# Kernel tuning notes

Hardware: AMD Instinct MI355X
Metric: run time of the kernel (lower is better)

## Reference

```python
import jax, jax.numpy as jnp
import numpy as np

S1 = (42, 1600, 1408); S2 = (21, 800, 704); S3 = (11, 400, 352); S4 = (6, 200, 176)
OFF = np.array([[dz, dy, dx] for dz in (-1, 0, 1) for dy in (-1, 0, 1) for dx in (-1, 0, 1)], np.int64)
KOFF = np.array([[kz, ky, kx] for kz in (0, 1, 2) for ky in (0, 1, 2) for kx in (0, 1, 2)], np.int64)

def _keys(c, s):
    return (c[:, 0] * s[1] + c[:, 1]) * s[2] + c[:, 2]

def _lookup(skeys, qk, valid):
    pos = np.searchsorted(skeys, qk)
    posc = np.clip(pos, 0, len(skeys) - 1)
    found = valid & (skeys[posc] == qk)
    return np.where(found, posc, -1).astype(np.int32)

def _subm_nbr(coords, skeys, shape):
    N = len(coords); nbr = np.empty((N, 27), np.int32); sh = np.array(shape)
    for t in range(27):
        q = coords + OFF[t]
        valid = np.all((q >= 0) & (q < sh), axis=1)
        nbr[:, t] = _lookup(skeys, _keys(q, shape), valid)
    return nbr

def _inv_nbr(fcoords, ckeys, cshape):
    # inverse of stride-2, pad-1, k-3 sparse conv: coarse = (fine + 1 - k) / 2
    N = len(fcoords); nbr = np.empty((N, 27), np.int32); csh = np.array(cshape)
    for t in range(27):
        cand = fcoords + 1 - KOFF[t]
        valid = np.all(cand >= 0, axis=1) & np.all(cand % 2 == 0, axis=1)
        cc = cand // 2
        valid &= np.all(cc < csh, axis=1)
        nbr[:, t] = _lookup(ckeys, _keys(cc, cshape), valid)
    return nbr

def _geometry():
    rng = np.random.default_rng(0)
    n = 130000
    c = np.stack([rng.integers(0, S1[i], n) for i in range(3)], 1).astype(np.int64)
    uk, idx = np.unique(_keys(c, S1), return_index=True)
    c1 = c[idx][:100000]; k1 = uk[:len(c1)]
    def down(cf, s):
        cc = cf // 2
        uk, idx = np.unique(_keys(cc, s), return_index=True)
        return cc[idx], uk
    c2, k2 = down(c1, S2); c3, k3 = down(c2, S3); c4, k4 = down(c3, S4)
    return dict(nbr4=_subm_nbr(c4, k4, S4), inv43=_inv_nbr(c3, k4, S4),
                nbr3=_subm_nbr(c3, k3, S3), inv32=_inv_nbr(c2, k3, S3),
                nbr2=_subm_nbr(c2, k2, S2), inv21=_inv_nbr(c1, k2, S2),
                nbr1=_subm_nbr(c1, k1, S1), n4=len(c4), n1=len(c1))

_SPECS = [("m4", 64, 64), ("i4", 64, 64), ("m3", 64, 64), ("i3", 64, 32),
          ("m2", 32, 32), ("i2", 32, 16), ("m1", 16, 16), ("c5", 16, 3)]

def _params(key):
    p = {}
    for i, (nm, ci, co) in enumerate(_SPECS):
        k = jax.random.fold_in(key, i)
        p["W_" + nm] = jax.random.normal(k, (27, ci, co), jnp.float32) * (1.0 / np.sqrt(27.0 * ci))
        p["g_" + nm] = jnp.ones((co,), jnp.float32)
        p["b_" + nm] = jnp.zeros((co,), jnp.float32)
    return p

def setup_inputs() -> dict:
    geo = _geometry()
    key = jax.random.key(0)
    inp = {k: jnp.asarray(v) for k, v in geo.items() if k.startswith(("nbr", "inv"))}
    inp["x"] = jax.random.normal(jax.random.fold_in(key, 100), (geo["n4"], 64), jnp.float32)
    inp.update(_params(key))
    return inp

def _block(f, nbr, W, g, b, relu=True):
    # gather-GEMM (sparse conv), then BatchNorm1d (training mode, eps=1e-3), then ReLU
    m = nbr >= 0                                             # [N,27]
    x = jnp.where(m[..., None], f[jnp.maximum(nbr, 0)], 0.0)  # [N,27,Cin]
    y = jnp.einsum('nkc,kcd->nd', x, W)                      # [N,Cout]
    mu = y.mean(0); var = y.var(0)
    y = (y - mu) * jax.lax.rsqrt(var + 1e-3) * g + b
    return jax.nn.relu(y) if relu else y

def reference(x, nbr4, inv43, nbr3, inv32, nbr2, inv21, nbr1,
              W_m4, g_m4, b_m4, W_i4, g_i4, b_i4, W_m3, g_m3, b_m3, W_i3, g_i3, b_i3,
              W_m2, g_m2, b_m2, W_i2, g_i2, b_i2, W_m1, g_m1, b_m1, W_c5, g_c5, b_c5):
    h = _block(x, nbr4, W_m4, g_m4, b_m4)      # subm4: [N4,64]
    h = _block(h, inv43, W_i4, g_i4, b_i4)     # inverse conv4 -> [N3,64]
    h = _block(h, nbr3, W_m3, g_m3, b_m3)      # subm3
    h = _block(h, inv32, W_i3, g_i3, b_i3)     # inverse conv3 -> [N2,32]
    h = _block(h, nbr2, W_m2, g_m2, b_m2)      # subm2
    h = _block(h, inv21, W_i2, g_i2, b_i2)     # inverse conv2 -> [N1,16]
    h = _block(h, nbr1, W_m1, g_m1, b_m1)      # subm1
    return _block(h, nbr1, W_c5, g_c5, b_c5, relu=False)  # conv5 (shares subm1 rulebook), BN only
```

## Files before the change

### kernel.cpp

```cpp
#include <hip/hip_runtime.h>

typedef _Float16 HALF;
typedef _Float16 f16x8 __attribute__((ext_vector_type(8)));
typedef float f32x4 __attribute__((ext_vector_type(4)));
typedef int i32x4 __attribute__((ext_vector_type(4)));

struct WArgs { const float* W[8]; HALF* dst[8]; };

__global__ void convert_all_w_kernel(WArgs a)
{
    const int CIs[8]  = {64, 64, 64, 64, 32, 32, 16, 16};
    const int COs[8]  = {64, 64, 64, 32, 32, 16, 16, 3};
    const int COPs[8] = {64, 64, 64, 32, 32, 16, 16, 16};
    const int L = blockIdx.y;
    const int CI = CIs[L], CO = COs[L], COP = COPs[L];
    const int K = 27 * CI, KP = (K + 31) & ~31;
    const int total = COP * KP;
    for (int i = blockIdx.x * 256 + threadIdx.x; i < total; i += gridDim.x * 256) {
        int jp = i / KP;
        int kp = i - jp * KP;
        float v = (jp < CO && kp < K) ? a.W[L][(size_t)kp * CO + jp] : 0.f;
        a.dst[L][((size_t)(kp >> 5) * COP + jp) * 32 + (kp & 31)] = (HALF)v;
    }
}

__global__ void convert_x_kernel(const float* __restrict__ x, HALF* __restrict__ xh, int total)
{
    int i = blockIdx.x * 256 + threadIdx.x;
    if (i < total) xh[i] = (HALF)x[i];
}

template<int CO_PAD, bool FUSED>
__global__ __launch_bounds__(256, 2) void conv_static(
    const HALF* __restrict__ h, const int* __restrict__ nbr,
    const HALF* __restrict__ Wt, HALF* __restrict__ yout,
    float* __restrict__ sums, int n,
    const float* __restrict__ psums, const float* __restrict__ pg,
    const float* __restrict__ pb, float pinvn)
{
    constexpr int CI   = 64;
    constexpr int NMT  = 2;
    constexpr int NJB  = CO_PAD / 16;
    constexpr int NCB  = 2;
    constexpr int ROWS = 32;
    constexpr int PAIRS = NMT * NJB;
    constexpr int TPW  = 7;

    __shared__ f32x4 lred[2][PAIRS * 64];
    __shared__ float lscbi[2][64];

    const int wv   = threadIdx.x >> 6;
    const int lane = threadIdx.x & 63;
    const int l15  = lane & 15;
    const int lq   = lane >> 4;

    int bid = blockIdx.x;
    {
        const int nwg = gridDim.x;
        const int q = nwg >> 3, r = nwg & 7;
        const int xcd = bid & 7, idx = bid >> 3;
        bid = (xcd < r ? xcd * (q + 1) : r * (q + 1) + (xcd - r) * q) + idx;
    }
    const int rowBase = bid * ROWS;

    if constexpr (FUSED) {
        const int c = threadIdx.x;
        if (c < CI) {
            float s = 0.f, q = 0.f;
#pragma unroll
            for (int k = 0; k < 8; ++k) { s += psums[k * 128 + c]; q += psums[k * 128 + CI + c]; }
            const float mu  = s * pinvn;
            const float var = q * pinvn - mu * mu;
            const float sc  = rsqrtf(var + 1e-3f) * pg[c];
            lscbi[0][c] = sc;
            lscbi[1][c] = pb[c] - mu * sc;
        }
    }

    f32x4 acc[NMT][NJB];
#pragma unroll
    for (int mt = 0; mt < NMT; ++mt)
#pragma unroll
        for (int jb = 0; jb < NJB; ++jb)
#pragma unroll
            for (int r = 0; r < 4; ++r) acc[mt][jb][r] = 0.f;

    int  nbo[NMT];
    bool rok[NMT];
#pragma unroll
    for (int mt = 0; mt < NMT; ++mt) {
        const int row = rowBase + mt * 16 + l15;
        rok[mt] = row < n;
        nbo[mt] = min(row, n - 1) * 27;
    }

    if constexpr (FUSED) __syncthreads();

    f16x8 sc8[NCB], bi8[NCB];
    if constexpr (FUSED) {
#pragma unroll
        for (int cb = 0; cb < NCB; ++cb) {
            const int c0 = cb * 32 + ((lq * 8) & (CI - 1));
#pragma unroll
            for (int j = 0; j < 8; ++j) {
                sc8[cb][j] = (HALF)lscbi[0][c0 + j];
                bi8[cb][j] = (HALF)lscbi[1][c0 + j];
            }
        }
    }

    const int t0 = wv * TPW;

    int   ipf[2][NMT];
    f16x8 apf[2][NMT][2];
#pragma unroll
    for (int p = 0; p < 2; ++p) {
        const int t = t0 + p;
#pragma unroll
        for (int mt = 0; mt < NMT; ++mt) {
            const int v   = nbr[nbo[mt] + (t < 27 ? t : 26)];
            const int idx = (rok[mt] && t < 27) ? v : -1;
            ipf[p][mt] = idx;
            const HALF* pa = h + ((max(idx, 0) << 6) + lq * 8);
            apf[p][mt][0] = *(const f16x8*)(pa);
            apf[p][mt][1] = *(const f16x8*)(pa + 32);
        }
    }

#pragma unroll
    for (int tt = 0; tt < TPW; ++tt) {
        const int t = t0 + tt;
        if (t >= 27) break;
        const int cur = tt & 1;

        f16x8 a0[NMT], a1[NMT]; int im[NMT];
#pragma unroll
        for (int mt = 0; mt < NMT; ++mt) {
            a0[mt] = apf[cur][mt][0]; a1[mt] = apf[cur][mt][1]; im[mt] = ipf[cur][mt];
        }

        if (tt + 2 < TPW && t + 2 < 27) {
#pragma unroll
            for (int mt = 0; mt < NMT; ++mt) {
                const int v   = nbr[nbo[mt] + t + 2];
                const int idx = rok[mt] ? v : -1;
                ipf[cur][mt] = idx;
                const HALF* pa = h + ((max(idx, 0) << 6) + lq * 8);
                apf[cur][mt][0] = *(const f16x8*)(pa);
                apf[cur][mt][1] = *(const f16x8*)(pa + 32);
            }
        }

        const HALF* wb = Wt + (size_t)(2 * t) * (CO_PAD * 32) + lq * 8;
        f16x8 b0[NJB], b1[NJB];
#pragma unroll
        for (int jb = 0; jb < NJB; ++jb) {
            b0[jb] = *(const f16x8*)(wb + (size_t)(jb * 16 + l15) * 32);
            b1[jb] = *(const f16x8*)(wb + CO_PAD * 32 + (size_t)(jb * 16 + l15) * 32);
        }

#pragma unroll
        for (int mt = 0; mt < NMT; ++mt) {
            f16x8 a = a0[mt];
            if constexpr (FUSED) {
                a = a * sc8[0] + bi8[0];
#pragma unroll
                for (int j = 0; j < 8; ++j) a[j] = (a[j] < (HALF)0.f) ? (HALF)0.f : a[j];
            }
            const int m = ~(im[mt] >> 31);
            i32x4 ai = __builtin_bit_cast(i32x4, a);
            ai.x &= m; ai.y &= m; ai.z &= m; ai.w &= m;
            a = __builtin_bit_cast(f16x8, ai);
#pragma unroll
            for (int jb = 0; jb < NJB; ++jb)
                acc[mt][jb] = __builtin_amdgcn_mfma_f32_16x16x32_f16(a, b0[jb], acc[mt][jb], 0, 0, 0);
        }
#pragma unroll
        for (int mt = 0; mt < NMT; ++mt) {
            f16x8 a = a1[mt];
            if constexpr (FUSED) {
                a = a * sc8[1] + bi8[1];
#pragma unroll
                for (int j = 0; j < 8; ++j) a[j] = (a[j] < (HALF)0.f) ? (HALF)0.f : a[j];
            }
            const int m = ~(im[mt] >> 31);
            i32x4 ai = __builtin_bit_cast(i32x4, a);
            ai.x &= m; ai.y &= m; ai.z &= m; ai.w &= m;
            a = __builtin_bit_cast(f16x8, ai);
#pragma unroll
            for (int jb = 0; jb < NJB; ++jb)
                acc[mt][jb] = __builtin_amdgcn_mfma_f32_16x16x32_f16(a, b1[jb], acc[mt][jb], 0, 0, 0);
        }
    }

    if (wv & 1) {
#pragma unroll
        for (int mt = 0; mt < NMT; ++mt)
#pragma unroll
            for (int jb = 0; jb < NJB; ++jb)
                lred[wv >> 1][(mt * NJB + jb) * 64 + lane] = acc[mt][jb];
    }
    __syncthreads();
    if (!(wv & 1)) {
#pragma unroll
        for (int mt = 0; mt < NMT; ++mt)
#pragma unroll
            for (int jb = 0; jb < NJB; ++jb)
                acc[mt][jb] += lred[wv >> 1][(mt * NJB + jb) * 64 + lane];
    }
    __syncthreads();
    if (wv == 2) {
#pragma unroll
        for (int mt = 0; mt < NMT; ++mt)
#pragma unroll
            for (int jb = 0; jb < NJB; ++jb)
                lred[0][(mt * NJB + jb) * 64 + lane] = acc[mt][jb];
    }
    __syncthreads();

    if (wv == 0) {
#pragma unroll
        for (int mt = 0; mt < NMT; ++mt)
#pragma unroll
            for (int jb = 0; jb < NJB; ++jb)
                acc[mt][jb] += lred[0][(mt * NJB + jb) * 64 + lane];

        float* sl = sums + (bid & 7) * 128;
#pragma unroll
        for (int jb = 0; jb < NJB; ++jb) {
            const int col = jb * 16 + l15;
            float s = 0.f, sq = 0.f;
#pragma unroll
            for (int mt = 0; mt < NMT; ++mt) {
                const int rb = rowBase + mt * 16 + lq * 4;
#pragma unroll
                for (int r = 0; r < 4; ++r) {
                    if (rb + r < n) {
                        const float v = acc[mt][jb][r];
                        yout[(size_t)(rb + r) * CO_PAD + col] = (HALF)v;
                        s += v;
                        sq += v * v;
                    }
                }
            }
            s  += __shfl_xor(s, 16);  s  += __shfl_xor(s, 32);
            sq += __shfl_xor(sq, 16); sq += __shfl_xor(sq, 32);
            if (lane < 16) {
                atomicAdd(&sl[col], s);
                atomicAdd(&sl[CO_PAD + col], sq);
            }
        }
    }
}

template<int CI, int CO_PAD, bool FUSED>
__global__ __launch_bounds__(256, 2) void conv_dyn(
    const HALF* __restrict__ h, const int* __restrict__ nbr,
    const HALF* __restrict__ Wt, HALF* __restrict__ yout,
    float* __restrict__ sums, int n,
    const float* __restrict__ psums, const float* __restrict__ pg,
    const float* __restrict__ pb, float pinvn)
{
    constexpr int NMT   = 2;
    constexpr int NJB   = CO_PAD / 16;
    constexpr int NCB   = (CI >= 64) ? 2 : 1;
    constexpr int ROWS  = 32;
    constexpr int PAIRS = NMT * NJB;

    __shared__ f32x4 lred[2][PAIRS * 64];
    __shared__ float lscbi[2][64];
    __shared__ int   lidx[ROWS * 27];
    __shared__ int   tflag[27];
    __shared__ int   tls[32];
    __shared__ int   ntapS;

    const int wv   = threadIdx.x >> 6;
    const int lane = threadIdx.x & 63;
    const int l15  = lane & 15;
    const int lq   = lane >> 4;

    int bid = blockIdx.x;
    {
        const int nwg = gridDim.x;
        const int q = nwg >> 3, r = nwg & 7;
        const int xcd = bid & 7, idx = bid >> 3;
        bid = (xcd < r ? xcd * (q + 1) : r * (q + 1) + (xcd - r) * q) + idx;
    }
    const int rowBase = bid * ROWS;

    for (int i = threadIdx.x; i < ROWS * 27; i += 256) {
        const int r   = i / 27;
        const int row = rowBase + r;
        lidx[i] = (row < n) ? nbr[(size_t)row * 27 + (i - r * 27)] : -1;
    }
    if constexpr (FUSED) {
        const int c = threadIdx.x;
        if (c < CI) {
            float s = 0.f, q = 0.f;
#pragma unroll
            for (int k = 0; k < 8; ++k) { s += psums[k * 128 + c]; q += psums[k * 128 + CI + c]; }
            const float mu  = s * pinvn;
            const float var = q * pinvn - mu * mu;
            const float sc  = rsqrtf(var + 1e-3f) * pg[c];
            lscbi[0][c] = sc;
            lscbi[1][c] = pb[c] - mu * sc;
        }
    }
    __syncthreads();

    if (threadIdx.x < 27) {
        int any = 0;
        for (int r = 0; r < ROWS; ++r) any |= ~(lidx[r * 27 + threadIdx.x] >> 31);
        tflag[threadIdx.x] = any & 1;
    }
    __syncthreads();
    if (threadIdx.x == 0) {
        int c = 0;
#pragma unroll
        for (int t = 0; t < 27; ++t) if (tflag[t]) tls[c++] = t;
        ntapS = c;
        for (int t = c; t < 32; ++t) tls[t] = 27;
    }
    __syncthreads();
    const int NT = ntapS;

    f16x8 sc8[NCB], bi8[NCB];
    if constexpr (FUSED) {
#pragma unroll
        for (int cb = 0; cb < NCB; ++cb) {
            const int c0 = cb * 32 + ((lq * 8) & (CI - 1));
#pragma unroll
            for (int j = 0; j < 8; ++j) {
                sc8[cb][j] = (HALF)lscbi[0][c0 + j];
                bi8[cb][j] = (HALF)lscbi[1][c0 + j];
            }
        }
    }

    f32x4 acc[NMT][NJB];
#pragma unroll
    for (int mt = 0; mt < NMT; ++mt)
#pragma unroll
        for (int jb = 0; jb < NJB; ++jb)
#pragma unroll
            for (int r = 0; r < 4; ++r) acc[mt][jb][r] = 0.f;

    int lb[NMT];
#pragma unroll
    for (int mt = 0; mt < NMT; ++mt) lb[mt] = (mt * 16 + l15) * 27;

    #define CONSUME(aV_, imV_, bV_, CBIDX_) do { \
        f16x8 a_ = (aV_); \
        if constexpr (FUSED) { \
            a_ = a_ * sc8[CBIDX_] + bi8[CBIDX_]; \
            _Pragma("unroll") \
            for (int j_ = 0; j_ < 8; ++j_) a_[j_] = (a_[j_] < (HALF)0.f) ? (HALF)0.f : a_[j_]; \
        } \
        const int m_ = ~((imV_) >> 31); \
        i32x4 ai_ = __builtin_bit_cast(i32x4, a_); \
        ai_.x &= m_; ai_.y &= m_; ai_.z &= m_; ai_.w &= m_; \
        a_ = __builtin_bit_cast(f16x8, ai_); \
        _Pragma("unroll") \
        for (int jb_ = 0; jb_ < NJB; ++jb_) \
            acc[mt][jb_] = __builtin_amdgcn_mfma_f32_16x16x32_f16(a_, (bV_)[jb_], acc[mt][jb_], 0, 0, 0); \
    } while (0)

    if constexpr (CI == 64) {
        int ti = wv;
        int   tcur, icur[NMT];
        f16x8 a0c[NMT], a1c[NMT];
        {
            tcur = tls[ti];
#pragma unroll
            for (int mt = 0; mt < NMT; ++mt) {
                const int idx = (tcur < 27) ? lidx[lb[mt] + min(tcur, 26)] : -1;
                icur[mt] = idx;
                const HALF* pa = h + ((max(idx, 0) << 6) + lq * 8);
                a0c[mt] = *(const f16x8*)(pa);
                a1c[mt] = *(const f16x8*)(pa + 32);
            }
        }
        for (; ti < NT; ti += 4) {
            int   tnx = tls[min(ti + 4, 31)];
            int   inx[NMT];
            f16x8 a0n[NMT], a1n[NMT];
#pragma unroll
            for (int mt = 0; mt < NMT; ++mt) {
                const int idx = (tnx < 27) ? lidx[lb[mt] + min(tnx, 26)] : -1;
                inx[mt] = idx;
                const HALF* pa = h + ((max(idx, 0) << 6) + lq * 8);
                a0n[mt] = *(const f16x8*)(pa);
                a1n[mt] = *(const f16x8*)(pa + 32);
            }

            const HALF* wb = Wt + (size_t)(2 * tcur) * (CO_PAD * 32) + lq * 8;
            f16x8 b0[NJB], b1[NJB];
#pragma unroll
            for (int jb = 0; jb < NJB; ++jb) {
                b0[jb] = *(const f16x8*)(wb + (size_t)(jb * 16 + l15) * 32);
                b1[jb] = *(const f16x8*)(wb + CO_PAD * 32 + (size_t)(jb * 16 + l15) * 32);
            }

#pragma unroll
            for (int mt = 0; mt < NMT; ++mt) CONSUME(a0c[mt], icur[mt], b0, 0);
#pragma unroll
            for (int mt = 0; mt < NMT; ++mt) CONSUME(a1c[mt], icur[mt], b1, NCB - 1);

            tcur = tnx;
#pragma unroll
            for (int mt = 0; mt < NMT; ++mt) {
                icur[mt] = inx[mt]; a0c[mt] = a0n[mt]; a1c[mt] = a1n[mt];
            }
        }
    } else if constexpr (CI == 32) {
        int ti = wv;
        int   tcur, icur[NMT];
        f16x8 ac[NMT];
        {
            tcur = tls[ti];
#pragma unroll
            for (int mt = 0; mt < NMT; ++mt) {
                const int idx = (tcur < 27) ? lidx[lb[mt] + min(tcur, 26)] : -1;
                icur[mt] = idx;
                ac[mt] = *(const f16x8*)(h + ((max(idx, 0) << 5) + lq * 8));
            }
        }
        for (; ti < NT; ti += 4) {
            int   tnx = tls[min(ti + 4, 31)];
            int   inx[NMT];
            f16x8 an[NMT];
#pragma unroll
            for (int mt = 0; mt < NMT; ++mt) {
                const int idx = (tnx < 27) ? lidx[lb[mt] + min(tnx, 26)] : -1;
                inx[mt] = idx;
                an[mt] = *(const f16x8*)(h + ((max(idx, 0) << 5) + lq * 8));
            }

            const HALF* wb = Wt + (size_t)tcur * (CO_PAD * 32) + lq * 8;
            f16x8 b[NJB];
#pragma unroll
            for (int jb = 0; jb < NJB; ++jb)
                b[jb] = *(const f16x8*)(wb + (size_t)(jb * 16 + l15) * 32);

#pragma unroll
            for (int mt = 0; mt < NMT; ++mt) CONSUME(ac[mt], icur[mt], b, 0);

            tcur = tnx;
#pragma unroll
            for (int mt = 0; mt < NMT; ++mt) { icur[mt] = inx[mt]; ac[mt] = an[mt]; }
        }
    } else {
        const int NS = (NT + 1) >> 1;
        int ti = wv;
        int   tcur, icur[NMT];
        f16x8 ac[NMT];
        {
            tcur = tls[min(2 * ti + (lq >> 1), 31)];
#pragma unroll
            for (int mt = 0; mt < NMT; ++mt) {
                const int idx = (tcur < 27) ? lidx[lb[mt] + min(tcur, 26)] : -1;
                icur[mt] = idx;
                ac[mt] = *(const f16x8*)(h + ((max(idx, 0) << 4) + (lq & 1) * 8));
            }
        }
        for (; ti < NS; ti += 4) {
            int   tnx = tls[min(2 * (ti + 4) + (lq >> 1), 31)];
            int   inx[NMT];
            f16x8 an[NMT];
#pragma unroll
            for (int mt = 0; mt < NMT; ++mt) {
                const int idx = (tnx < 27) ? lidx[lb[mt] + min(tnx, 26)] : -1;
                inx[mt] = idx;
                an[mt] = *(const f16x8*)(h + ((max(idx, 0) << 4) + (lq & 1) * 8));
            }

            const int tb = min(tcur, 26);
            f16x8 b[NJB];
#pragma unroll
            for (int jb = 0; jb < NJB; ++jb)
                b[jb] = *(const f16x8*)(Wt + (size_t)(tb >> 1) * (CO_PAD * 32)
                                        + (size_t)(jb * 16 + l15) * 32 + (tb & 1) * 16 + (lq & 1) * 8);

#pragma unroll
            for (int mt = 0; mt < NMT; ++mt) CONSUME(ac[mt], icur[mt], b, 0);

            tcur = tnx;
#pragma unroll
            for (int mt = 0; mt < NMT; ++mt) { icur[mt] = inx[mt]; ac[mt] = an[mt]; }
        }
    }
    #undef CONSUME

    if (wv & 1) {
#pragma unroll
        for (int mt = 0; mt < NMT; ++mt)
#pragma unroll
            for (int jb = 0; jb < NJB; ++jb)
                lred[wv >> 1][(mt * NJB + jb) * 64 + lane] = acc[mt][jb];
    }
    __syncthreads();
    if (!(wv & 1)) {
#pragma unroll
        for (int mt = 0; mt < NMT; ++mt)
#pragma unroll
            for (int jb = 0; jb < NJB; ++jb)
                acc[mt][jb] += lred[wv >> 1][(mt * NJB + jb) * 64 + lane];
    }
    __syncthreads();
    if (wv == 2) {
#pragma unroll
        for (int mt = 0; mt < NMT; ++mt)
#pragma unroll
            for (int jb = 0; jb < NJB; ++jb)
                lred[0][(mt * NJB + jb) * 64 + lane] = acc[mt][jb];
    }
    __syncthreads();

    if (wv == 0) {
#pragma unroll
        for (int mt = 0; mt < NMT; ++mt)
#pragma unroll
            for (int jb = 0; jb < NJB; ++jb)
                acc[mt][jb] += lred[0][(mt * NJB + jb) * 64 + lane];

        float* sl = sums + (bid & 7) * 128;
#pragma unroll
        for (int jb = 0; jb < NJB; ++jb) {
            const int col = jb * 16 + l15;
            float s = 0.f, sq = 0.f;
#pragma unroll
            for (int mt = 0; mt < NMT; ++mt) {
                const int rb = rowBase + mt * 16 + lq * 4;
#pragma unroll
                for (int r = 0; r < 4; ++r) {
                    if (rb + r < n) {
                        const float v = acc[mt][jb][r];
                        yout[(size_t)(rb + r) * CO_PAD + col] = (HALF)v;
                        s += v;
                        sq += v * v;
                    }
                }
            }
            s  += __shfl_xor(s, 16);  s  += __shfl_xor(s, 32);
            sq += __shfl_xor(sq, 16); sq += __shfl_xor(sq, 32);
            if (lane < 16) {
                atomicAdd(&sl[col], s);
                atomicAdd(&sl[CO_PAD + col], sq);
            }
        }
    }
}

__global__ void bn_out_kernel(const HALF* __restrict__ y, const float* __restrict__ sums,
                              const float* __restrict__ g, const float* __restrict__ b,
                              int n, float invn, float* __restrict__ out)
{
    int i = blockIdx.x * 256 + threadIdx.x;
    if (i >= n * 3) return;
    int row = i / 3;
    int c = i - row * 3;
    float ssum = 0.f, qsum = 0.f;
#pragma unroll
    for (int k2 = 0; k2 < 8; ++k2) {
        ssum += sums[k2 * 128 + c];
        qsum += sums[k2 * 128 + 16 + c];
    }
    float mu  = ssum * invn;
    float var = qsum * invn - mu * mu;
    float sc  = rsqrtf(var + 1e-3f) * g[c];
    out[i] = ((float)y[(size_t)row * 16 + c] - mu) * sc + b[c];
}

extern "C" void kernel_launch(void* const* d_in, const int* in_sizes, int n_in,
                              void* d_out, int out_size, void* d_ws, size_t ws_size,
                              hipStream_t stream)
{
    const int* nbr4  = (const int*)d_in[0];
    const int* inv43 = (const int*)d_in[1];
    const int* nbr3  = (const int*)d_in[2];
    const int* inv32 = (const int*)d_in[3];
    const int* nbr2  = (const int*)d_in[4];
    const int* inv21 = (const int*)d_in[5];
    const int* nbr1  = (const int*)d_in[6];
    const float* x   = (const float*)d_in[7];

    const int n4 = in_sizes[0] / 27;
    const int n3 = in_sizes[1] / 27;
    const int n2 = in_sizes[3] / 27;
    const int n1 = in_sizes[5] / 27;

    const int CIs[8]  = {64, 64, 64, 64, 32, 32, 16, 16};
    const int COPs[8] = {64, 64, 64, 32, 32, 16, 16, 16};
    int KPs[8], wtoff[8];
    int wtot = 0;
    for (int s = 0; s < 8; ++s) {
        KPs[s] = ((27 * CIs[s] + 31) / 32) * 32;
        wtoff[s] = wtot;
        wtot += COPs[s] * KPs[s];
    }

    char* ws = (char*)d_ws;
    HALF* wt = (HALF*)ws;
    size_t off = ((size_t)wtot * sizeof(HALF) + 255) & ~(size_t)255;
    float* sums = (float*)(ws + off);
    off += 8 * 1024 * sizeof(float);
    off = (off + 255) & ~(size_t)255;
    HALF* xh = (HALF*)(ws + off);
    off += ((size_t)n4 * 64 * sizeof(HALF) + 255) & ~(size_t)255;
    size_t bufElems = 0;
    {
        size_t cand[4] = {(size_t)n4 * 64, (size_t)n3 * 64, (size_t)n2 * 32, (size_t)n1 * 16};
        for (int i = 0; i < 4; ++i) if (cand[i] > bufElems) bufElems = cand[i];
    }
    HALF* Y0 = (HALF*)(ws + off);
    off += (bufElems * sizeof(HALF) + 255) & ~(size_t)255;
    HALF* Y1 = (HALF*)(ws + off);

    hipMemsetAsync(sums, 0, 8 * 1024 * sizeof(float), stream);

    WArgs wa;
    for (int s = 0; s < 8; ++s) { wa.W[s] = (const float*)d_in[8 + 3 * s]; wa.dst[s] = wt + wtoff[s]; }
    {
        int maxTotal = 64 * KPs[0];
        dim3 grid((maxTotal + 255) / 256, 8);
        convert_all_w_kernel<<<grid, 256, 0, stream>>>(wa);
    }
    convert_x_kernel<<<(n4 * 64 + 255) / 256, 256, 0, stream>>>(x, xh, n4 * 64);

#define G(s) ((const float*)d_in[9 + 3 * (s)])
#define B(s) ((const float*)d_in[10 + 3 * (s)])
#define SUMS(s) (sums + (s) * 1024)
#define GRID(nn) (((nn) + 31) / 32)

    conv_static<64, false><<<GRID(n4), 256, 0, stream>>>(
        xh, nbr4, wt + wtoff[0], Y0, SUMS(0), n4, nullptr, nullptr, nullptr, 0.f);
    conv_static<64, true><<<GRID(n3), 256, 0, stream>>>(
        Y0, inv43, wt + wtoff[1], Y1, SUMS(1), n3, SUMS(0), G(0), B(0), 1.f / n4);
    conv_static<64, true><<<GRID(n3), 256, 0, stream>>>(
        Y1, nbr3, wt + wtoff[2], Y0, SUMS(2), n3, SUMS(1), G(1), B(1), 1.f / n3);
    conv_dyn<64, 32, true><<<GRID(n2), 256, 0, stream>>>(
        Y0, inv32, wt + wtoff[3], Y1, SUMS(3), n2, SUMS(2), G(2), B(2), 1.f / n3);
    conv_dyn<32, 32, true><<<GRID(n2), 256, 0, stream>>>(
        Y1, nbr2, wt + wtoff[4], Y0, SUMS(4), n2, SUMS(3), G(3), B(3), 1.f / n2);
    conv_dyn<32, 16, true><<<GRID(n1), 256, 0, stream>>>(
        Y0, inv21, wt + wtoff[5], Y1, SUMS(5), n1, SUMS(4), G(4), B(4), 1.f / n2);
    conv_dyn<16, 16, true><<<GRID(n1), 256, 0, stream>>>(
        Y1, nbr1, wt + wtoff[6], Y0, SUMS(6), n1, SUMS(5), G(5), B(5), 1.f / n1);
    conv_dyn<16, 16, true><<<GRID(n1), 256, 0, stream>>>(
        Y0, nbr1, wt + wtoff[7], Y1, SUMS(7), n1, SUMS(6), G(6), B(6), 1.f / n1);
    bn_out_kernel<<<(n1 * 3 + 255) / 256, 256, 0, stream>>>(
        Y1, SUMS(7), G(7), B(7), n1, 1.f / n1, (float*)d_out);

#undef G
#undef B
#undef SUMS
#undef GRID
}
```

Baseline: 462.6 us.

## Stage contiguous neighbor bands in LDS for 64-channel sparse conv layers

Replaces the per-thread gather-with-register-prefetch kernel for the first three 64-channel layers with a banded version. Each block loads its 32x27 rulebook into LDS, finds the min/max neighbor index for each of the 9 (dz,dy) groups, and when the span fits 128 rows it copies that contiguous slab of features into double-buffered LDS, then gathers from LDS. Waves are re-split by row tile and channel half instead of by kernel offset. The aim is to exploit spatial locality of sorted voxel indices so global loads become coalesced. The cost is extra barriers per group, about 40KB of LDS per block, lost register prefetch, and a fallback to global gathers when the span is wide.

```diff
diff --git a/kernel.cpp b/kernel.cpp
--- a/kernel.cpp
+++ b/kernel.cpp
@@ -31,28 +31,31 @@
 }
 
 template<int CO_PAD, bool FUSED>
-__global__ __launch_bounds__(256, 2) void conv_static(
+__global__ __launch_bounds__(256, 2) void conv_band(
     const HALF* __restrict__ h, const int* __restrict__ nbr,
     const HALF* __restrict__ Wt, HALF* __restrict__ yout,
     float* __restrict__ sums, int n,
     const float* __restrict__ psums, const float* __restrict__ pg,
     const float* __restrict__ pb, float pinvn)
 {
-    constexpr int CI   = 64;
-    constexpr int NMT  = 2;
-    constexpr int NJB  = CO_PAD / 16;
-    constexpr int NCB  = 2;
-    constexpr int ROWS = 32;
-    constexpr int PAIRS = NMT * NJB;
-    constexpr int TPW  = 7;
-
-    __shared__ f32x4 lred[2][PAIRS * 64];
+    constexpr int CI    = 64;
+    constexpr int NJB   = CO_PAD / 16;
+    constexpr int ROWS  = 32;
+    constexpr int BMAX  = 128;
+    constexpr int RPAD  = 72;
+
     __shared__ float lscbi[2][64];
+    __shared__ int   lidx[ROWS * 27];
+    __shared__ int   glo[9], ghi[9];
+    __shared__ HALF  band[2][BMAX * RPAD];
+    __shared__ f32x4 lred[2][NJB * 64];
 
     const int wv   = threadIdx.x >> 6;
     const int lane = threadIdx.x & 63;
     const int l15  = lane & 15;
     const int lq   = lane >> 4;
+    const int mt   = wv & 1;
+    const int kh   = wv >> 1;
 
     int bid = blockIdx.x;
     {
@@ -63,6 +66,11 @@
     }
     const int rowBase = bid * ROWS;
 
+    for (int i = threadIdx.x; i < ROWS * 27; i += 256) {
+        const int r   = i / 27;
+        const int row = rowBase + r;
+        lidx[i] = (row < n) ? nbr[(size_t)row * 27 + (i - r * 27)] : -1;
+    }
     if constexpr (FUSED) {
         const int c = threadIdx.x;
         if (c < CI) {
@@ -76,171 +84,136 @@
             lscbi[1][c] = pb[c] - mu * sc;
         }
     }
-
-    f32x4 acc[NMT][NJB];
-#pragma unroll
-    for (int mt = 0; mt < NMT; ++mt)
+    if (threadIdx.x < 9) { glo[threadIdx.x] = 0x7fffffff; ghi[threadIdx.x] = -1; }
+    __syncthreads();
+
+    if (threadIdx.x < 216) {
+        const int g = threadIdx.x / 24, j = threadIdx.x % 24;
+        int mn = 0x7fffffff, mx = -1;
+#pragma unroll
+        for (int e = j * 4; e < j * 4 + 4; ++e) {
+            const int r = e / 3, t = g * 3 + e % 3;
+            const int v = lidx[r * 27 + t];
+            if (v >= 0) { mn = min(mn, v); mx = max(mx, v); }
+        }
+        if (mx >= 0) { atomicMin(&glo[g], mn); atomicMax(&ghi[g], mx); }
+    }
+    __syncthreads();
+
+    f16x8 sc8, bi8;
+    if constexpr (FUSED) {
+        const int c0 = kh * 32 + lq * 8;
+#pragma unroll
+        for (int j = 0; j < 8; ++j) { sc8[j] = (HALF)lscbi[0][c0 + j]; bi8[j] = (HALF)lscbi[1][c0 + j]; }
+    }
+
+    f32x4 acc[NJB];
+#pragma unroll
+    for (int jb = 0; jb < NJB; ++jb)
+#pragma unroll
+        for (int r = 0; r < 4; ++r) acc[jb][r] = 0.f;
+
+    const int lbase = (mt * 16 + l15) * 27;
+
+    #define LOADBAND(g_, buf_) do { \
+        const int lo_ = glo[g_]; \
+        const int W_  = ghi[g_] - lo_ + 1; \
+        for (int u = threadIdx.x; u < W_ * 8; u += 256) { \
+            const int rr_ = u >> 3, ck_ = u & 7; \
+            const i32x4 v_ = *(const i32x4*)(h + (size_t)(lo_ + rr_) * 64 + ck_ * 8); \
+            *(i32x4*)(&band[buf_][rr_ * RPAD + ck_ * 8]) = v_; \
+        } \
+    } while (0)
+
+    #define CONSUME(aV_, imV_, bV_) do { \
+        f16x8 a_ = (aV_); \
+        if constexpr (FUSED) { \
+            a_ = a_ * sc8 + bi8; \
+            _Pragma("unroll") \
+            for (int j_ = 0; j_ < 8; ++j_) a_[j_] = (a_[j_] < (HALF)0.f) ? (HALF)0.f : a_[j_]; \
+        } \
+        const int m_ = ~((imV_) >> 31); \
+        i32x4 ai_ = __builtin_bit_cast(i32x4, a_); \
+        ai_.x &= m_; ai_.y &= m_; ai_.z &= m_; ai_.w &= m_; \
+        a_ = __builtin_bit_cast(f16x8, ai_); \
+        _Pragma("unroll") \
+        for (int jb_ = 0; jb_ < NJB; ++jb_) \
+            acc[jb_] = __builtin_amdgcn_mfma_f32_16x16x32_f16(a_, (bV_)[jb_], acc[jb_], 0, 0, 0); \
+    } while (0)
+
+    #define GMODE(g_) ((ghi[g_] < 0) ? 0 : ((ghi[g_] - glo[g_] + 1 <= BMAX) ? 1 : 2))
+
+    if (GMODE(0) == 1) LOADBAND(0, 0);
+    __syncthreads();
+
+    for (int g = 0; g < 9; ++g) {
+        if (g + 1 < 9 && GMODE(g + 1) == 1) LOADBAND(g + 1, (g + 1) & 1);
+
+        const int gm = GMODE(g);
+        if (gm == 1) {
+            const int lo = glo[g];
+            const HALF* bb = &band[g & 1][0];
+#pragma unroll
+            for (int dxi = 0; dxi < 3; ++dxi) {
+                const int t   = g * 3 + dxi;
+                const int idx = lidx[lbase + t];
+                const int off = max(idx, lo) - lo;
+                const f16x8 a = *(const f16x8*)(bb + off * RPAD + kh * 32 + lq * 8);
+
+                const HALF* wb = Wt + (size_t)(2 * t + kh) * (CO_PAD * 32) + lq * 8;
+                f16x8 b[NJB];
+#pragma unroll
+                for (int jb = 0; jb < NJB; ++jb)
+                    b[jb] = *(const f16x8*)(wb + (size_t)(jb * 16 + l15) * 32);
+
+                CONSUME(a, idx, b);
+            }
+        } else if (gm == 2) {
+#pragma unroll
+            for (int dxi = 0; dxi < 3; ++dxi) {
+                const int t   = g * 3 + dxi;
+                const int idx = lidx[lbase + t];
+                const f16x8 a = *(const f16x8*)(h + ((size_t)max(idx, 0) << 6) + kh * 32 + lq * 8);
+
+                const HALF* wb = Wt + (size_t)(2 * t + kh) * (CO_PAD * 32) + lq * 8;
+                f16x8 b[NJB];
+#pragma unroll
+                for (int jb = 0; jb < NJB; ++jb)
+                    b[jb] = *(const f16x8*)(wb + (size_t)(jb * 16 + l15) * 32);
+
+                CONSUME(a, idx, b);
+            }
+        }
+        __syncthreads();
+    }
+    #undef GMODE
+    #undef CONSUME
+    #undef LOADBAND
+
+    if (kh == 1) {
 #pragma unroll
         for (int jb = 0; jb < NJB; ++jb)
-#pragma unroll
-            for (int r = 0; r < 4; ++r) acc[mt][jb][r] = 0.f;
-
-    int  nbo[NMT];
-    bool rok[NMT];
-#pragma unroll
-    for (int mt = 0; mt < NMT; ++mt) {
-        const int row = rowBase + mt * 16 + l15;
-        rok[mt] = row < n;
-        nbo[mt] = min(row, n - 1) * 27;
-    }
-
-    if constexpr (FUSED) __syncthreads();
-
-    f16x8 sc8[NCB], bi8[NCB];
-    if constexpr (FUSED) {
-#pragma unroll
-        for (int cb = 0; cb < NCB; ++cb) {
-            const int c0 = cb * 32 + ((lq * 8) & (CI - 1));
-#pragma unroll
-            for (int j = 0; j < 8; ++j) {
-                sc8[cb][j] = (HALF)lscbi[0][c0 + j];
-                bi8[cb][j] = (HALF)lscbi[1][c0 + j];
-            }
-        }
-    }
-
-    const int t0 = wv * TPW;
-
-    int   ipf[2][NMT];
-    f16x8 apf[2][NMT][2];
-#pragma unroll
-    for (int p = 0; p < 2; ++p) {
-        const int t = t0 + p;
-#pragma unroll
-        for (int mt = 0; mt < NMT; ++mt) {
-            const int v   = nbr[nbo[mt] + (t < 27 ? t : 26)];
-            const int idx = (rok[mt] && t < 27) ? v : -1;
-            ipf[p][mt] = idx;
-            const HALF* pa = h + ((max(idx, 0) << 6) + lq * 8);
-            apf[p][mt][0] = *(const f16x8*)(pa);
-            apf[p][mt][1] = *(const f16x8*)(pa + 32);
-        }
-    }
-
-#pragma unroll
-    for (int tt = 0; tt < TPW; ++tt) {
-        const int t = t0 + tt;
-        if (t >= 27) break;
-        const int cur = tt & 1;
-
-        f16x8 a0[NMT], a1[NMT]; int im[NMT];
-#pragma unroll
-        for (int mt = 0; mt < NMT; ++mt) {
-            a0[mt] = apf[cur][mt][0]; a1[mt] = apf[cur][mt][1]; im[mt] = ipf[cur][mt];
-        }
-
-        if (tt + 2 < TPW && t + 2 < 27) {
-#pragma unroll
-            for (int mt = 0; mt < NMT; ++mt) {
-                const int v   = nbr[nbo[mt] + t + 2];
-                const int idx = rok[mt] ? v : -1;
-                ipf[cur][mt] = idx;
-                const HALF* pa = h + ((max(idx, 0) << 6) + lq * 8);
-                apf[cur][mt][0] = *(const f16x8*)(pa);
-                apf[cur][mt][1] = *(const f16x8*)(pa + 32);
-            }
-        }
-
-        const HALF* wb = Wt + (size_t)(2 * t) * (CO_PAD * 32) + lq * 8;
-        f16x8 b0[NJB], b1[NJB];
-#pragma unroll
-        for (int jb = 0; jb < NJB; ++jb) {
-            b0[jb] = *(const f16x8*)(wb + (size_t)(jb * 16 + l15) * 32);
-            b1[jb] = *(const f16x8*)(wb + CO_PAD * 32 + (size_t)(jb * 16 + l15) * 32);
-        }
-
-#pragma unroll
-        for (int mt = 0; mt < NMT; ++mt) {
-            f16x8 a = a0[mt];
-            if constexpr (FUSED) {
-                a = a * sc8[0] + bi8[0];
-#pragma unroll
-                for (int j = 0; j < 8; ++j) a[j] = (a[j] < (HALF)0.f) ? (HALF)0.f : a[j];
-            }
-            const int m = ~(im[mt] >> 31);
-            i32x4 ai = __builtin_bit_cast(i32x4, a);
-            ai.x &= m; ai.y &= m; ai.z &= m; ai.w &= m;
-            a = __builtin_bit_cast(f16x8, ai);
-#pragma unroll
-            for (int jb = 0; jb < NJB; ++jb)
-                acc[mt][jb] = __builtin_amdgcn_mfma_f32_16x16x32_f16(a, b0[jb], acc[mt][jb], 0, 0, 0);
-        }
-#pragma unroll
-        for (int mt = 0; mt < NMT; ++mt) {
-            f16x8 a = a1[mt];
-            if constexpr (FUSED) {
-                a = a * sc8[1] + bi8[1];
-#pragma unroll
-                for (int j = 0; j < 8; ++j) a[j] = (a[j] < (HALF)0.f) ? (HALF)0.f : a[j];
-            }
-            const int m = ~(im[mt] >> 31);
-            i32x4 ai = __builtin_bit_cast(i32x4, a);
-            ai.x &= m; ai.y &= m; ai.z &= m; ai.w &= m;
-            a = __builtin_bit_cast(f16x8, ai);
-#pragma unroll
-            for (int jb = 0; jb < NJB; ++jb)
-                acc[mt][jb] = __builtin_amdgcn_mfma_f32_16x16x32_f16(a, b1[jb], acc[mt][jb], 0, 0, 0);
-        }
-    }
-
-    if (wv & 1) {
-#pragma unroll
-        for (int mt = 0; mt < NMT; ++mt)
-#pragma unroll
-            for (int jb = 0; jb < NJB; ++jb)
-                lred[wv >> 1][(mt * NJB + jb) * 64 + lane] = acc[mt][jb];
-    }
-    __syncthreads();
-    if (!(wv & 1)) {
-#pragma unroll
-        for (int mt = 0; mt < NMT; ++mt)
-#pragma unroll
-            for (int jb = 0; jb < NJB; ++jb)
-                acc[mt][jb] += lred[wv >> 1][(mt * NJB + jb) * 64 + lane];
-    }
-    __syncthreads();
-    if (wv == 2) {
-#pragma unroll
-        for (int mt = 0; mt < NMT; ++mt)
-#pragma unroll
-            for (int jb = 0; jb < NJB; ++jb)
-                lred[0][(mt * NJB + jb) * 64 + lane] = acc[mt][jb];
-    }
-    __syncthreads();
-
-    if (wv == 0) {
-#pragma unroll
-        for (int mt = 0; mt < NMT; ++mt)
-#pragma unroll
-            for (int jb = 0; jb < NJB; ++jb)
-                acc[mt][jb] += lred[0][(mt * NJB + jb) * 64 + lane];
+            lred[mt][jb * 64 + lane] = acc[jb];
+    }
+    __syncthreads();
+    if (kh == 0) {
+#pragma unroll
+        for (int jb = 0; jb < NJB; ++jb)
+            acc[jb] += lred[mt][jb * 64 + lane];
 
         float* sl = sums + (bid & 7) * 128;
 #pragma unroll
         for (int jb = 0; jb < NJB; ++jb) {
             const int col = jb * 16 + l15;
             float s = 0.f, sq = 0.f;
-#pragma unroll
-            for (int mt = 0; mt < NMT; ++mt) {
-                const int rb = rowBase + mt * 16 + lq * 4;
-#pragma unroll
-                for (int r = 0; r < 4; ++r) {
-                    if (rb + r < n) {
-                        const float v = acc[mt][jb][r];
-                        yout[(size_t)(rb + r) * CO_PAD + col] = (HALF)v;
-                        s += v;
-                        sq += v * v;
-                    }
+            const int rb = rowBase + mt * 16 + lq * 4;
+#pragma unroll
+            for (int r = 0; r < 4; ++r) {
+                if (rb + r < n) {
+                    const float v = acc[jb][r];
+                    yout[(size_t)(rb + r) * CO_PAD + col] = (HALF)v;
+                    s += v;
+                    sq += v * v;
                 }
             }
             s  += __shfl_xor(s, 16);  s  += __shfl_xor(s, 32);
@@ -632,11 +605,11 @@
 #define SUMS(s) (sums + (s) * 1024)
 #define GRID(nn) (((nn) + 31) / 32)
 
-    conv_static<64, false><<<GRID(n4), 256, 0, stream>>>(
+    conv_band<64, false><<<GRID(n4), 256, 0, stream>>>(
         xh, nbr4, wt + wtoff[0], Y0, SUMS(0), n4, nullptr, nullptr, nullptr, 0.f);
-    conv_static<64, true><<<GRID(n3), 256, 0, stream>>>(
+    conv_band<64, true><<<GRID(n3), 256, 0, stream>>>(
         Y0, inv43, wt + wtoff[1], Y1, SUMS(1), n3, SUMS(0), G(0), B(0), 1.f / n4);
-    conv_static<64, true><<<GRID(n3), 256, 0, stream>>>(
+    conv_band<64, true><<<GRID(n3), 256, 0, stream>>>(
         Y1, nbr3, wt + wtoff[2], Y0, SUMS(2), n3, SUMS(1), G(1), B(1), 1.f / n3);
     conv_dyn<64, 32, true><<<GRID(n2), 256, 0, stream>>>(
         Y0, inv32, wt + wtoff[3], Y1, SUMS(3), n2, SUMS(2), G(2), B(2), 1.f / n3);
```

Result: slower. 542.0 us (+17.2%).
